# Kernel optimization log

Hardware: AMD Instinct MI355X
Metric: run time of the kernel (lower is better)

The kernel has to match this reference:

```python
import jax, jax.numpy as jnp
import numpy as np

B, DIM, RES, NS, ITERS = 64, 256, 32, 8, 5
NTOK = RES * RES
HID = max(DIM, 128)
EPS = 1e-08
SCALE = DIM ** -0.5


def build_grid(res):
    r = [np.linspace(0.0, 1.0, num=n) for n in (res, res)]
    g = np.stack(np.meshgrid(*r, sparse=False, indexing='ij'), axis=-1)
    g = g.reshape(1, res, res, 2).astype(np.float32)
    return jnp.asarray(np.concatenate([g, 1.0 - g], axis=-1))  # [1,res,res,4]


def ln(x, g, b, eps=1e-5):
    m = x.mean(-1, keepdims=True)
    v = ((x - m) ** 2).mean(-1, keepdims=True)
    return (x - m) / jnp.sqrt(v + eps) * g + b


def ln2(x, g, b, eps=1e-5):  # LayerNorm over last two dims ([ntokens, dim])
    m = x.mean((-2, -1), keepdims=True)
    v = ((x - m) ** 2).mean((-2, -1), keepdims=True)
    return (x - m) / jnp.sqrt(v + eps) * g + b


def lin(x, W, b):
    return x @ W.T + b


def gru_cell(x, h, W_ih, W_hh, b_ih, b_hh):
    gi = x @ W_ih.T + b_ih
    gh = h @ W_hh.T + b_hh
    ir, iz, i_n = jnp.split(gi, 3, axis=-1)
    hr, hz, h_n = jnp.split(gh, 3, axis=-1)
    r = jax.nn.sigmoid(ir + hr)
    z = jax.nn.sigmoid(iz + hz)
    n = jnp.tanh(i_n + r * h_n)
    return (1.0 - z) * n + z * h


def setup_inputs() -> dict:
    key = jax.random.key(0)
    ks = jax.random.split(key, 32)
    p = lambda i, shape, s=0.02: (jax.random.normal(ks[i], shape, dtype=jnp.float32) * s)
    d = {
        'inputs': jax.random.normal(ks[0], (B, DIM, RES, RES), dtype=jnp.float32),
        'init_noise': jax.random.normal(ks[1], (B, NS, DIM), dtype=jnp.float32),
        'W_pos': p(2, (DIM, 4)), 'b_pos': jnp.zeros((DIM,)),
        'g_enc': jnp.ones((NTOK, DIM)), 'b_enc': jnp.zeros((NTOK, DIM)),
        'W_m1': p(3, (DIM, DIM)), 'b_m1': jnp.zeros((DIM,)),
        'W_m2': p(4, (DIM, DIM)), 'b_m2': jnp.zeros((DIM,)),
        'g_in': jnp.ones((DIM,)), 'b_in': jnp.zeros((DIM,)),
        'Wq': p(5, (DIM, DIM)), 'bq': jnp.zeros((DIM,)),
        'Wk': p(6, (DIM, DIM)), 'bk': jnp.zeros((DIM,)),
        'Wv': p(7, (DIM, DIM)), 'bv': jnp.zeros((DIM,)),
        'W_ih': p(8, (3 * DIM, DIM)), 'W_hh': p(9, (3 * DIM, DIM)),
        'b_ih': jnp.zeros((3 * DIM,)), 'b_hh': jnp.zeros((3 * DIM,)),
        'g_s': jnp.ones((DIM,)), 'b_s': jnp.zeros((DIM,)),
        'g_ff': jnp.ones((DIM,)), 'b_ff': jnp.zeros((DIM,)),
        'W_f1': p(10, (HID, DIM)), 'b_f1': jnp.zeros((HID,)),
        'W_f2': p(11, (DIM, HID)), 'b_f2': jnp.zeros((DIM,)),
        'mu': p(12, (1, 1, DIM), 0.1), 'sigma': p(13, (1, 1, DIM), 0.1),
    }
    return d


def _forward(inputs, init_noise, W_pos, b_pos, g_enc, b_enc, W_m1, b_m1, W_m2, b_m2,
             g_in, b_in, Wq, bq, Wk, bk, Wv, bv, W_ih, W_hh, b_ih, b_hh,
             g_s, b_s, g_ff, b_ff, W_f1, b_f1, W_f2, b_f2, mu, sigma):
    grid = build_grid(RES)  # [1,RES,RES,4]
    # encoder transformation (position=True)
    f = jnp.transpose(inputs, (0, 2, 3, 1))               # [B,RES,RES,DIM]
    f = f + lin(grid, W_pos, b_pos)                       # soft position embed
    f = f.reshape(B, NTOK, DIM)
    f = ln2(f, g_enc, b_enc)                              # LayerNorm([ntokens, dim])
    f = jnp.maximum(lin(f, W_m1, b_m1), 0.0)
    f = jnp.maximum(lin(f, W_m2, b_m2), 0.0)
    f = ln(f, g_in, b_in)                                 # norm_input
    k = lin(f, Wk, bk)
    v = lin(f, Wv, bv)

    def step(slots):
        s = ln(slots, g_s, b_s)
        q = lin(s, Wq, bq)
        dots = jnp.einsum('bid,bjd->bij', q, k) * SCALE   # [B,NS,NTOK]
        attn = jax.nn.softmax(dots, axis=1) + EPS         # softmax over slots
        attn = attn / attn.sum(-1, keepdims=True)         # weighted mean
        upd = jnp.einsum('bij,bjd->bid', attn, v)
        ns = gru_cell(upd.reshape(-1, DIM), slots.reshape(-1, DIM),
                      W_ih, W_hh, b_ih, b_hh).reshape(B, NS, DIM)
        h = jnp.maximum(lin(ln(ns, g_ff, b_ff), W_f1, b_f1), 0.0)
        return ns + lin(h, W_f2, b_f2)

    slots = mu + sigma * init_noise
    for _ in range(ITERS):
        slots = step(slots)
    # implicit differentiation: one extra step through detached slots
    slots = step(jax.lax.stop_gradient(slots))
    return slots


def reference(inputs, init_noise, W_pos, b_pos, g_enc, b_enc, W_m1, b_m1, W_m2, b_m2,
              g_in, b_in, Wq, bq, Wk, bk, Wv, bv, W_ih, W_hh, b_ih, b_hh,
              g_s, b_s, g_ff, b_ff, W_f1, b_f1, W_f2, b_f2, mu, sigma):
    return _forward(inputs, init_noise, W_pos, b_pos, g_enc, b_enc, W_m1, b_m1, W_m2, b_m2,
                    g_in, b_in, Wq, bq, Wk, bk, Wv, bv, W_ih, W_hh, b_ih, b_hh,
                    g_s, b_s, g_ff, b_ff, W_f1, b_f1, W_f2, b_f2, mu, sigma)
```

## Files before the change

kernel.cpp:

```cpp
#include <hip/hip_runtime.h>
#include <hip/hip_bf16.h>

#define BB    64
#define DIMN  256
#define NSLOT 8
#define NTOKN 1024
#define NSTEP 6
#define SCALEF 0.0625f

typedef __attribute__((ext_vector_type(8))) short short8;
typedef __attribute__((ext_vector_type(8))) unsigned short ushort8;
typedef __attribute__((ext_vector_type(4))) unsigned short ushort4v;
typedef __attribute__((ext_vector_type(4))) float f32x4;

__device__ __forceinline__ float b2f(unsigned short u) {
  return __uint_as_float((unsigned)u << 16);
}
__device__ __forceinline__ unsigned short f2b(float f) {
  unsigned u = __float_as_uint(f);
  return (unsigned short)((u + 0x7FFFu + ((u >> 16) & 1u)) >> 16);
}

constexpr int kNConv = 31;
constexpr int kConvSizes[kNConv] = {
  131072, 1024, 256, 262144, 262144, 65536, 256, 65536, 256, 256, 256,
  65536, 256, 65536, 256, 65536, 256, 196608, 196608, 768, 768,
  256, 256, 256, 256, 65536, 256, 65536, 256, 256, 256
};
constexpr int kConvTotal = 1513984;

struct PtrPack { const void* p[kNConv]; };

__device__ __forceinline__ float ldin(const void* p, long i, int isbf) {
  if (isbf) return b2f(((const unsigned short*)p)[i]);
  return ((const float*)p)[i];
}

__global__ void detect_dtype(const void* gin, int* flag) {
  unsigned u = *(const unsigned*)gin;
  *flag = (u == 0x3F803F80u) ? 1 : 0;
}

__global__ __launch_bounds__(256) void convert_weights(PtrPack pk, const int* __restrict__ flag,
                                                       float* __restrict__ dst) {
  int idx = blockIdx.x * 256 + threadIdx.x;
  if (idx >= kConvTotal) return;
  int off = idx, a = 0;
  while (a < kNConv - 1 && off >= kConvSizes[a]) { off -= kConvSizes[a]; ++a; }
  dst[idx] = ldin(pk.p[a], off, *flag);
}

constexpr int kWN = 9;
constexpr int kWSize[kWN]  = {65536, 65536, 65536, 65536, 65536, 196608, 196608, 65536, 65536};
constexpr int kWSrc[kWN]   = {656640, 722432, 788736, 854528, 920320, 986112, 1182720, 1381888, 1447680};
constexpr int kWTotal = 851968;

__global__ __launch_bounds__(256) void convert_wbf16(const float* __restrict__ conv,
                                                     unsigned short* __restrict__ wbf) {
  int idx = blockIdx.x * 256 + threadIdx.x;
  if (idx >= kWTotal) return;
  int off = idx, m = 0;
  while (m < kWN - 1 && off >= kWSize[m]) { off -= kWSize[m]; ++m; }
  wbf[idx] = f2b(conv[kWSrc[m] + off]);
}

__global__ __launch_bounds__(256) void posembed_stats(
    const void* __restrict__ in0, const int* __restrict__ flag,
    const float* __restrict__ Wpos, const float* __restrict__ bpos,
    unsigned short* __restrict__ A, float* __restrict__ partials) {
  __shared__ float lds[64 * 65];
  __shared__ float red[8];
  const int tb = blockIdx.x, b = blockIdx.y, tid = threadIdx.x;
  const int t0 = tb * 64;
  const int isbf = *flag;
  float sum = 0.f, ss = 0.f;
  const int tg = tid & 7;
  const int dbase = tid >> 3;
  const int tloc = tg * 8;
  const int dq = tid & 15;
  const int trow = tid >> 4;
  for (int d0 = 0; d0 < DIMN; d0 += 64) {
    __syncthreads();
#pragma unroll
    for (int p = 0; p < 2; ++p) {
      int dd = dbase + p * 32;
      int d = d0 + dd;
      const float* wp = Wpos + d * 4;
      int tf = t0 + tloc;
      float gi = (float)(tf >> 5) * (1.f / 31.f);
      float gj0 = (float)(tf & 31) * (1.f / 31.f);
      float base = wp[0] * gi + wp[2] * (1.f - gi) + wp[1] * gj0 + wp[3] * (1.f - gj0) + bpos[d];
      float step = (wp[1] - wp[3]) * (1.f / 31.f);
      long gidx = ((long)b * DIMN + d) * NTOKN + tf;
      float v[8];
      if (isbf) {
        ushort8 raw = *(const ushort8*)((const unsigned short*)in0 + gidx);
#pragma unroll
        for (int j = 0; j < 8; ++j) v[j] = b2f(raw[j]);
      } else {
        const float* fp = (const float*)in0 + gidx;
        float4 a0 = *(const float4*)fp;
        float4 a1 = *(const float4*)(fp + 4);
        v[0] = a0.x; v[1] = a0.y; v[2] = a0.z; v[3] = a0.w;
        v[4] = a1.x; v[5] = a1.y; v[6] = a1.z; v[7] = a1.w;
      }
#pragma unroll
      for (int j = 0; j < 8; ++j) {
        float val = v[j] + base + step * (float)j;
        sum += val; ss += val * val;
        lds[dd * 65 + tloc + j] = val;
      }
    }
    __syncthreads();
#pragma unroll
    for (int p = 0; p < 4; ++p) {
      int tt = trow + p * 16;
      int dcol = dq * 4;
      ushort4v y;
      y[0] = f2b(lds[(dcol + 0) * 65 + tt]);
      y[1] = f2b(lds[(dcol + 1) * 65 + tt]);
      y[2] = f2b(lds[(dcol + 2) * 65 + tt]);
      y[3] = f2b(lds[(dcol + 3) * 65 + tt]);
      *(ushort4v*)(A + ((long)b * NTOKN + t0 + tt) * DIMN + d0 + dcol) = y;
    }
  }
  for (int off = 32; off; off >>= 1) { sum += __shfl_xor(sum, off); ss += __shfl_xor(ss, off); }
  int w = tid >> 6;
  if ((tid & 63) == 0) { red[w] = sum; red[4 + w] = ss; }
  __syncthreads();
  if (tid == 0) {
    partials[((long)b * 16 + tb) * 2]     = red[0] + red[1] + red[2] + red[3];
    partials[((long)b * 16 + tb) * 2 + 1] = red[4] + red[5] + red[6] + red[7];
  }
}

__global__ void stats_reduce(const float* __restrict__ partials, float* __restrict__ stats) {
  int b = threadIdx.x;
  if (b >= BB) return;
  float s = 0.f, q = 0.f;
  for (int i = 0; i < 16; ++i) {
    s += partials[((long)b * 16 + i) * 2];
    q += partials[((long)b * 16 + i) * 2 + 1];
  }
  const float invN = 1.f / (float)(NTOKN * DIMN);
  float m = s * invN;
  float var = q * invN - m * m;
  stats[b * 2] = m;
  stats[b * 2 + 1] = rsqrtf(var + 1e-5f);
}

__global__ __launch_bounds__(256) void ln2_apply(unsigned short* __restrict__ A, const float* __restrict__ stats,
                                                 const float* __restrict__ genc, const float* __restrict__ benc) {
  long i8 = (long)blockIdx.x * 256 + threadIdx.x;
  long i = i8 * 8;
  int b = (int)(i >> 18);
  int td = (int)(i & 262143);
  float m = stats[b * 2], inv = stats[b * 2 + 1];
  ushort8 x = *(const ushort8*)(A + i);
  ushort8 y;
#pragma unroll
  for (int e = 0; e < 8; ++e) {
    float v = (b2f(x[e]) - m) * inv * genc[td + e] + benc[td + e];
    y[e] = f2b(v);
  }
  *(ushort8*)(A + i) = y;
}

__global__ __launch_bounds__(256) void rowln_bf(const unsigned short* __restrict__ X,
                                                const float* __restrict__ g, const float* __restrict__ bb,
                                                unsigned short* __restrict__ Y) {
  const int tid = threadIdx.x, lane = tid & 63;
  const long row = (long)blockIdx.x * 4 + (tid >> 6);
  ushort4v xv = *(const ushort4v*)(X + row * 256 + lane * 4);
  float x0 = b2f(xv[0]), x1 = b2f(xv[1]), x2 = b2f(xv[2]), x3 = b2f(xv[3]);
  float s = x0 + x1 + x2 + x3;
  float q = x0 * x0 + x1 * x1 + x2 * x2 + x3 * x3;
  for (int off = 32; off; off >>= 1) { s += __shfl_xor(s, off); q += __shfl_xor(q, off); }
  float m = s * (1.f / 256.f);
  float inv = rsqrtf(q * (1.f / 256.f) - m * m + 1e-5f);
  float4 gv = *(const float4*)(g + lane * 4);
  float4 bv = *(const float4*)(bb + lane * 4);
  ushort4v y;
  y[0] = f2b((x0 - m) * inv * gv.x + bv.x);
  y[1] = f2b((x1 - m) * inv * gv.y + bv.y);
  y[2] = f2b((x2 - m) * inv * gv.z + bv.z);
  y[3] = f2b((x3 - m) * inv * gv.w + bv.w);
  *(ushort4v*)(Y + row * 256 + lane * 4) = y;
}

template <int ACT, int OUT>
__global__ __launch_bounds__(256) void gemm_tile(
    const unsigned short* __restrict__ X, const unsigned short* __restrict__ W,
    const float* __restrict__ bias, const float* __restrict__ res,
    void* __restrict__ Y, int Nfull) {
  __shared__ unsigned short As[128 * 264];
  __shared__ unsigned short Bs[128 * 264];
  const int tid = threadIdx.x;
  const long m0 = (long)blockIdx.x * 128;
  const int n0 = blockIdx.y * 128;
#pragma unroll
  for (int i = 0; i < 16; ++i) {
    int c = tid + i * 256;
    int row = c >> 5, seg = c & 31;
    *(ushort8*)&As[row * 264 + seg * 8] = *(const ushort8*)(X + (m0 + row) * 256 + seg * 8);
  }
#pragma unroll
  for (int i = 0; i < 16; ++i) {
    int c = tid + i * 256;
    int row = c >> 5, seg = c & 31;
    *(ushort8*)&Bs[row * 264 + seg * 8] = *(const ushort8*)(W + (long)(n0 + row) * 256 + seg * 8);
  }
  __syncthreads();
  const int wave = tid >> 6, lane = tid & 63;
  const int wr = wave >> 1, wc = wave & 1;
  const int lrow = lane & 15, kgrp = lane >> 4;
  f32x4 acc[4][4];
#pragma unroll
  for (int mt = 0; mt < 4; ++mt)
#pragma unroll
    for (int nt = 0; nt < 4; ++nt) acc[mt][nt] = f32x4{0.f, 0.f, 0.f, 0.f};
#pragma unroll
  for (int kc = 0; kc < 8; ++kc) {
    short8 af[4], bf[4];
#pragma unroll
    for (int mt = 0; mt < 4; ++mt)
      af[mt] = *(const short8*)&As[(wr * 64 + mt * 16 + lrow) * 264 + kc * 32 + kgrp * 8];
#pragma unroll
    for (int nt = 0; nt < 4; ++nt)
      bf[nt] = *(const short8*)&Bs[(wc * 64 + nt * 16 + lrow) * 264 + kc * 32 + kgrp * 8];
#pragma unroll
    for (int mt = 0; mt < 4; ++mt)
#pragma unroll
      for (int nt = 0; nt < 4; ++nt)
        acc[mt][nt] = __builtin_amdgcn_mfma_f32_16x16x32_bf16(af[mt], bf[nt], acc[mt][nt], 0, 0, 0);
  }
#pragma unroll
  for (int mt = 0; mt < 4; ++mt)
#pragma unroll
    for (int nt = 0; nt < 4; ++nt) {
      int n = n0 + wc * 64 + nt * 16 + lrow;
      float bn = bias[n];
#pragma unroll
      for (int r = 0; r < 4; ++r) {
        long m = m0 + wr * 64 + mt * 16 + kgrp * 4 + r;
        float v = acc[mt][nt][r] + bn;
        if (ACT) v = fmaxf(v, 0.f);
        if (OUT == 0)      ((unsigned short*)Y)[m * Nfull + n] = f2b(v);
        else if (OUT == 1) ((float*)Y)[m * Nfull + n] = v;
        else               ((float*)Y)[m * Nfull + n] = v + res[m * Nfull + n];
      }
    }
}

__global__ __launch_bounds__(256) void gemm_kv_tile(
    const unsigned short* __restrict__ X,
    const unsigned short* __restrict__ Wk, const unsigned short* __restrict__ Wv,
    const float* __restrict__ bk, const float* __restrict__ bv,
    unsigned short* __restrict__ Kb, unsigned short* __restrict__ Vb) {
  __shared__ unsigned short As[128 * 264];
  __shared__ unsigned short Bs[128 * 264];
  const int tid = threadIdx.x;
  const long m0 = (long)blockIdx.x * 128;
  const int n0 = blockIdx.y * 128;
#pragma unroll
  for (int i = 0; i < 16; ++i) {
    int c = tid + i * 256;
    int row = c >> 5, seg = c & 31;
    *(ushort8*)&As[row * 264 + seg * 8] = *(const ushort8*)(X + (m0 + row) * 256 + seg * 8);
  }
  const int wave = tid >> 6, lane = tid & 63;
  const int wr = wave >> 1, wc = wave & 1;
  const int lrow = lane & 15, kgrp = lane >> 4;
  for (int which = 0; which < 2; ++which) {
    const unsigned short* W = which ? Wv : Wk;
    const float* bias = which ? bv : bk;
    unsigned short* Y = which ? Vb : Kb;
    if (which) __syncthreads();
#pragma unroll
    for (int i = 0; i < 16; ++i) {
      int c = tid + i * 256;
      int row = c >> 5, seg = c & 31;
      *(ushort8*)&Bs[row * 264 + seg * 8] = *(const ushort8*)(W + (long)(n0 + row) * 256 + seg * 8);
    }
    __syncthreads();
    f32x4 acc[4][4];
#pragma unroll
    for (int mt = 0; mt < 4; ++mt)
#pragma unroll
      for (int nt = 0; nt < 4; ++nt) acc[mt][nt] = f32x4{0.f, 0.f, 0.f, 0.f};
#pragma unroll
    for (int kc = 0; kc < 8; ++kc) {
      short8 af[4], bf[4];
#pragma unroll
      for (int mt = 0; mt < 4; ++mt)
        af[mt] = *(const short8*)&As[(wr * 64 + mt * 16 + lrow) * 264 + kc * 32 + kgrp * 8];
#pragma unroll
      for (int nt = 0; nt < 4; ++nt)
        bf[nt] = *(const short8*)&Bs[(wc * 64 + nt * 16 + lrow) * 264 + kc * 32 + kgrp * 8];
#pragma unroll
      for (int mt = 0; mt < 4; ++mt)
#pragma unroll
        for (int nt = 0; nt < 4; ++nt)
          acc[mt][nt] = __builtin_amdgcn_mfma_f32_16x16x32_bf16(af[mt], bf[nt], acc[mt][nt], 0, 0, 0);
    }
#pragma unroll
    for (int mt = 0; mt < 4; ++mt)
#pragma unroll
      for (int nt = 0; nt < 4; ++nt) {
        int n = n0 + wc * 64 + nt * 16 + lrow;
        float bn = bias[n];
#pragma unroll
        for (int r = 0; r < 4; ++r) {
          long m = m0 + wr * 64 + mt * 16 + kgrp * 4 + r;
          Y[m * 256 + n] = f2b(acc[mt][nt][r] + bn);
        }
      }
  }
}

template <int ACT, int OUT>
__global__ __launch_bounds__(256) void gemm_tile64(
    const unsigned short* __restrict__ X, const unsigned short* __restrict__ W,
    const float* __restrict__ bias, const float* __restrict__ res,
    void* __restrict__ Y, int Nfull) {
  __shared__ unsigned short As[64 * 264];
  __shared__ unsigned short Bs[128 * 264];
  const int tid = threadIdx.x;
  const long m0 = (long)blockIdx.x * 64;
  const int n0 = blockIdx.y * 128;
#pragma unroll
  for (int i = 0; i < 8; ++i) {
    int c = tid + i * 256;
    int row = c >> 5, seg = c & 31;
    *(ushort8*)&As[row * 264 + seg * 8] = *(const ushort8*)(X + (m0 + row) * 256 + seg * 8);
  }
#pragma unroll
  for (int i = 0; i < 16; ++i) {
    int c = tid + i * 256;
    int row = c >> 5, seg = c & 31;
    *(ushort8*)&Bs[row * 264 + seg * 8] = *(const ushort8*)(W + (long)(n0 + row) * 256 + seg * 8);
  }
  __syncthreads();
  const int wave = tid >> 6, lane = tid & 63;
  const int lrow = lane & 15, kgrp = lane >> 4;
  f32x4 acc[8];
#pragma unroll
  for (int nt = 0; nt < 8; ++nt) acc[nt] = f32x4{0.f, 0.f, 0.f, 0.f};
#pragma unroll
  for (int kc = 0; kc < 8; ++kc) {
    short8 af = *(const short8*)&As[(wave * 16 + lrow) * 264 + kc * 32 + kgrp * 8];
#pragma unroll
    for (int nt = 0; nt < 8; ++nt) {
      short8 bf = *(const short8*)&Bs[(nt * 16 + lrow) * 264 + kc * 32 + kgrp * 8];
      acc[nt] = __builtin_amdgcn_mfma_f32_16x16x32_bf16(af, bf, acc[nt], 0, 0, 0);
    }
  }
#pragma unroll
  for (int nt = 0; nt < 8; ++nt) {
    int n = n0 + nt * 16 + lrow;
    float bn = bias[n];
#pragma unroll
    for (int r = 0; r < 4; ++r) {
      long m = m0 + wave * 16 + kgrp * 4 + r;
      float v = acc[nt][r] + bn;
      if (ACT) v = fmaxf(v, 0.f);
      if (OUT == 0)      ((unsigned short*)Y)[m * Nfull + n] = f2b(v);
      else if (OUT == 1) ((float*)Y)[m * Nfull + n] = v;
      else               ((float*)Y)[m * Nfull + n] = v + res[m * Nfull + n];
    }
  }
}

__global__ __launch_bounds__(256) void gigh_tile(
    const unsigned short* __restrict__ updb, const unsigned short* __restrict__ sbf,
    const unsigned short* __restrict__ Wih, const unsigned short* __restrict__ Whh,
    const float* __restrict__ bih, const float* __restrict__ bhh,
    float* __restrict__ gib, float* __restrict__ ghb) {
  const unsigned short* X = blockIdx.z ? sbf : updb;
  const unsigned short* W = blockIdx.z ? Whh : Wih;
  const float* bias = blockIdx.z ? bhh : bih;
  float* Y = blockIdx.z ? ghb : gib;
  __shared__ unsigned short As[128 * 264];
  __shared__ unsigned short Bs[128 * 264];
  const int tid = threadIdx.x;
  const long m0 = (long)blockIdx.x * 128;
  const int n0 = blockIdx.y * 128;
#pragma unroll
  for (int i = 0; i < 16; ++i) {
    int c = tid + i * 256;
    int row = c >> 5, seg = c & 31;
    *(ushort8*)&As[row * 264 + seg * 8] = *(const ushort8*)(X + (m0 + row) * 256 + seg * 8);
  }
#pragma unroll
  for (int i = 0; i < 16; ++i) {
    int c = tid + i * 256;
    int row = c >> 5, seg = c & 31;
    *(ushort8*)&Bs[row * 264 + seg * 8] = *(const ushort8*)(W + (long)(n0 + row) * 256 + seg * 8);
  }
  __syncthreads();
  const int wave = tid >> 6, lane = tid & 63;
  const int wr = wave >> 1, wc = wave & 1;
  const int lrow = lane & 15, kgrp = lane >> 4;
  f32x4 acc[4][4];
#pragma unroll
  for (int mt = 0; mt < 4; ++mt)
#pragma unroll
    for (int nt = 0; nt < 4; ++nt) acc[mt][nt] = f32x4{0.f, 0.f, 0.f, 0.f};
#pragma unroll
  for (int kc = 0; kc < 8; ++kc) {
    short8 af[4], bf[4];
#pragma unroll
    for (int mt = 0; mt < 4; ++mt)
      af[mt] = *(const short8*)&As[(wr * 64 + mt * 16 + lrow) * 264 + kc * 32 + kgrp * 8];
#pragma unroll
    for (int nt = 0; nt < 4; ++nt)
      bf[nt] = *(const short8*)&Bs[(wc * 64 + nt * 16 + lrow) * 264 + kc * 32 + kgrp * 8];
#pragma unroll
    for (int mt = 0; mt < 4; ++mt)
#pragma unroll
      for (int nt = 0; nt < 4; ++nt)
        acc[mt][nt] = __builtin_amdgcn_mfma_f32_16x16x32_bf16(af[mt], bf[nt], acc[mt][nt], 0, 0, 0);
  }
#pragma unroll
  for (int mt = 0; mt < 4; ++mt)
#pragma unroll
    for (int nt = 0; nt < 4; ++nt) {
      int n = n0 + wc * 64 + nt * 16 + lrow;
      float bn = bias[n];
#pragma unroll
      for (int r = 0; r < 4; ++r) {
        long m = m0 + wr * 64 + mt * 16 + kgrp * 4 + r;
        Y[m * 768 + n] = acc[mt][nt][r] + bn;
      }
    }
}

__global__ __launch_bounds__(256) void slots_init(const float* __restrict__ noise, const float* __restrict__ mu,
                                                  const float* __restrict__ sigma, float* __restrict__ slots) {
  long i = (long)blockIdx.x * 256 + threadIdx.x;
  int d = (int)(i & 255);
  slots[i] = mu[d] + sigma[d] * noise[i];
}

__global__ __launch_bounds__(256) void lnq_q(
    const float* __restrict__ slots, const float* __restrict__ gs, const float* __restrict__ bs,
    const unsigned short* __restrict__ Wq, const float* __restrict__ bq,
    unsigned short* __restrict__ qb, unsigned short* __restrict__ sbf) {
  __shared__ unsigned short S[16 * 264];
  const int b = blockIdx.x, tid = threadIdx.x;
  const int wave = tid >> 6, lane = tid & 63;
  for (int i = tid; i < 8 * 264; i += 256) S[8 * 264 + i] = 0;
#pragma unroll
  for (int rr = 0; rr < 2; ++rr) {
    int row = wave * 2 + rr;
    float4 xv = *(const float4*)(slots + ((long)b * 8 + row) * 256 + lane * 4);
    float s = xv.x + xv.y + xv.z + xv.w;
    float q = xv.x * xv.x + xv.y * xv.y + xv.z * xv.z + xv.w * xv.w;
    for (int off = 32; off; off >>= 1) { s += __shfl_xor(s, off); q += __shfl_xor(q, off); }
    float m = s * (1.f / 256.f);
    float inv = rsqrtf(q * (1.f / 256.f) - m * m + 1e-5f);
    float4 gv = *(const float4*)(gs + lane * 4);
    float4 bv = *(const float4*)(bs + lane * 4);
    ushort4v y, rb;
    y[0] = f2b((xv.x - m) * inv * gv.x + bv.x);
    y[1] = f2b((xv.y - m) * inv * gv.y + bv.y);
    y[2] = f2b((xv.z - m) * inv * gv.z + bv.z);
    y[3] = f2b((xv.w - m) * inv * gv.w + bv.w);
    rb[0] = f2b(xv.x); rb[1] = f2b(xv.y); rb[2] = f2b(xv.z); rb[3] = f2b(xv.w);
    *(ushort4v*)&S[row * 264 + lane * 4] = y;
    *(ushort4v*)(sbf + ((long)b * 8 + row) * 256 + lane * 4) = rb;
  }
  __syncthreads();
  const int lrow = lane & 15, kgrp = lane >> 4;
  short8 a[8];
#pragma unroll
  for (int kc = 0; kc < 8; ++kc)
    a[kc] = *(const short8*)&S[lrow * 264 + kc * 32 + kgrp * 8];
#pragma unroll
  for (int nt = 0; nt < 4; ++nt) {
    const int n = wave * 64 + nt * 16 + lrow;
    const unsigned short* wp = Wq + (long)n * 256 + kgrp * 8;
    f32x4 acc = {0.f, 0.f, 0.f, 0.f};
#pragma unroll
    for (int kc = 0; kc < 8; ++kc)
      acc = __builtin_amdgcn_mfma_f32_16x16x32_bf16(a[kc], *(const short8*)(wp + kc * 32), acc, 0, 0, 0);
    if (kgrp < 2) {
      float bn = bq[n];
#pragma unroll
      for (int r = 0; r < 4; ++r)
        qb[((long)b * 8 + kgrp * 4 + r) * 256 + n] = f2b(acc[r] + bn);
    }
  }
}

__global__ __launch_bounds__(256) void attn1b(
    const unsigned short* __restrict__ qb, const unsigned short* __restrict__ Kb,
    const unsigned short* __restrict__ Vb,
    float* __restrict__ upd_part, float* __restrict__ asum_part) {
  __shared__ unsigned short Ks[64 * 264];
  __shared__ unsigned short Qs[16 * 264];
  __shared__ float attnS[64 * 8];
  __shared__ float red[4 * 2048];
  const int jt = blockIdx.x, b = blockIdx.y, tid = threadIdx.x;
  const int wave = tid >> 6, lane = tid & 63;
#pragma unroll
  for (int i = 0; i < 8; ++i) {
    int c = tid + i * 256;
    int row = c >> 5, seg = c & 31;
    *(ushort8*)&Ks[row * 264 + seg * 8] =
        *(const ushort8*)(Kb + ((long)(b * NTOKN + jt * 64 + row)) * 256 + seg * 8);
  }
  {
    int row = tid >> 5, seg = tid & 31;
    *(ushort8*)&Qs[row * 264 + seg * 8] = *(const ushort8*)(qb + ((long)(b * 8 + row)) * 256 + seg * 8);
  }
  for (int i = tid; i < 8 * 264; i += 256) Qs[8 * 264 + i] = 0;
  __syncthreads();
  const int lrow = lane & 15, kgrp = lane >> 4;
  f32x4 acc = {0.f, 0.f, 0.f, 0.f};
#pragma unroll
  for (int kc = 0; kc < 8; ++kc) {
    short8 af = *(const short8*)&Ks[(wave * 16 + lrow) * 264 + kc * 32 + kgrp * 8];
    short8 qf = *(const short8*)&Qs[lrow * 264 + kc * 32 + kgrp * 8];
    acc = __builtin_amdgcn_mfma_f32_16x16x32_bf16(af, qf, acc, 0, 0, 0);
  }
  float t0[4], mx[4], e[4], sm[4];
#pragma unroll
  for (int r = 0; r < 4; ++r) { t0[r] = acc[r] * SCALEF; mx[r] = t0[r]; }
#pragma unroll
  for (int msk = 1; msk <= 4; msk <<= 1)
#pragma unroll
    for (int r = 0; r < 4; ++r) mx[r] = fmaxf(mx[r], __shfl_xor(mx[r], msk));
#pragma unroll
  for (int r = 0; r < 4; ++r) { e[r] = expf(t0[r] - mx[r]); sm[r] = e[r]; }
#pragma unroll
  for (int msk = 1; msk <= 4; msk <<= 1)
#pragma unroll
    for (int r = 0; r < 4; ++r) sm[r] += __shfl_xor(sm[r], msk);
  if (lrow < 8) {
#pragma unroll
    for (int r = 0; r < 4; ++r) {
      int jl = wave * 16 + kgrp * 4 + r;
      attnS[jl * 8 + lrow] = e[r] / sm[r] + 1e-8f;
    }
  }
  __syncthreads();
  {
    int s0 = wave * 2;
    float v0 = attnS[lane * 8 + s0], v1 = attnS[lane * 8 + s0 + 1];
    for (int off = 32; off; off >>= 1) { v0 += __shfl_xor(v0, off); v1 += __shfl_xor(v1, off); }
    if (lane == 0) {
      asum_part[((long)(b * 16 + jt)) * 8 + s0] = v0;
      asum_part[((long)(b * 16 + jt)) * 8 + s0 + 1] = v1;
    }
  }
  float au[8][4] = {};
  for (int jl = 0; jl < 16; ++jl) {
    int j = wave * 16 + jl;
    ushort4v v4 = *(const ushort4v*)(Vb + ((long)(b * NTOKN + jt * 64 + j)) * 256 + lane * 4);
    float v0 = b2f(v4[0]), v1 = b2f(v4[1]), v2 = b2f(v4[2]), v3 = b2f(v4[3]);
    float4 a01 = *(const float4*)&attnS[j * 8];
    float4 a23 = *(const float4*)&attnS[j * 8 + 4];
    float aw[8] = {a01.x, a01.y, a01.z, a01.w, a23.x, a23.y, a23.z, a23.w};
#pragma unroll
    for (int s = 0; s < 8; ++s) {
      au[s][0] += aw[s] * v0; au[s][1] += aw[s] * v1;
      au[s][2] += aw[s] * v2; au[s][3] += aw[s] * v3;
    }
  }
#pragma unroll
  for (int s = 0; s < 8; ++s)
    *(float4*)&red[wave * 2048 + s * 256 + lane * 4] = make_float4(au[s][0], au[s][1], au[s][2], au[s][3]);
  __syncthreads();
#pragma unroll
  for (int i = 0; i < 8; ++i) {
    int idx = tid + i * 256;
    float sum = red[idx] + red[2048 + idx] + red[4096 + idx] + red[6144 + idx];
    upd_part[((long)(b * 16 + jt)) * 2048 + idx] = sum;
  }
}

__global__ __launch_bounds__(256) void upd_reduce(
    const float* __restrict__ upd_part, const float* __restrict__ asum_part,
    unsigned short* __restrict__ updb) {
  const int bx = blockIdx.x;
  const int b = bx >> 3, s = bx & 7;
  const int tid = threadIdx.x;
  float as = 0.f;
#pragma unroll
  for (int jt = 0; jt < 16; ++jt) as += asum_part[((long)(b * 16 + jt)) * 8 + s];
  float sum = 0.f;
#pragma unroll
  for (int jt = 0; jt < 16; ++jt)
    sum += upd_part[((long)(b * 16 + jt)) * 2048 + s * 256 + tid];
  updb[((long)b * 8 + s) * 256 + tid] = f2b(sum / as);
}

__global__ __launch_bounds__(256) void gru_ln(const float* __restrict__ gi, const float* __restrict__ gh,
                                              const float* __restrict__ slots,
                                              const float* __restrict__ gff, const float* __restrict__ bff,
                                              float* __restrict__ ns, unsigned short* __restrict__ ffl) {
  const int tid = threadIdx.x, lane = tid & 63;
  const long row = (long)blockIdx.x * 4 + (tid >> 6);
  const int d = lane * 4;
  float4 i1 = *(const float4*)(gi + row * 768 + d);
  float4 i2 = *(const float4*)(gi + row * 768 + 256 + d);
  float4 i3 = *(const float4*)(gi + row * 768 + 512 + d);
  float4 h1 = *(const float4*)(gh + row * 768 + d);
  float4 h2 = *(const float4*)(gh + row * 768 + 256 + d);
  float4 h3 = *(const float4*)(gh + row * 768 + 512 + d);
  float4 sl = *(const float4*)(slots + row * 256 + d);
  float n4[4];
  float r, z, nn;
  r = 1.f / (1.f + expf(-(i1.x + h1.x))); z = 1.f / (1.f + expf(-(i2.x + h2.x)));
  nn = tanhf(i3.x + r * h3.x); n4[0] = (1.f - z) * nn + z * sl.x;
  r = 1.f / (1.f + expf(-(i1.y + h1.y))); z = 1.f / (1.f + expf(-(i2.y + h2.y)));
  nn = tanhf(i3.y + r * h3.y); n4[1] = (1.f - z) * nn + z * sl.y;
  r = 1.f / (1.f + expf(-(i1.z + h1.z))); z = 1.f / (1.f + expf(-(i2.z + h2.z)));
  nn = tanhf(i3.z + r * h3.z); n4[2] = (1.f - z) * nn + z * sl.z;
  r = 1.f / (1.f + expf(-(i1.w + h1.w))); z = 1.f / (1.f + expf(-(i2.w + h2.w)));
  nn = tanhf(i3.w + r * h3.w); n4[3] = (1.f - z) * nn + z * sl.w;
  *(float4*)(ns + row * 256 + d) = make_float4(n4[0], n4[1], n4[2], n4[3]);
  float s = n4[0] + n4[1] + n4[2] + n4[3];
  float q = n4[0] * n4[0] + n4[1] * n4[1] + n4[2] * n4[2] + n4[3] * n4[3];
  for (int off = 32; off; off >>= 1) { s += __shfl_xor(s, off); q += __shfl_xor(q, off); }
  float m = s * (1.f / 256.f);
  float inv = rsqrtf(q * (1.f / 256.f) - m * m + 1e-5f);
  float4 gv = *(const float4*)(gff + d);
  float4 bv = *(const float4*)(bff + d);
  ushort4v y;
  y[0] = f2b((n4[0] - m) * inv * gv.x + bv.x);
  y[1] = f2b((n4[1] - m) * inv * gv.y + bv.y);
  y[2] = f2b((n4[2] - m) * inv * gv.z + bv.z);
  y[3] = f2b((n4[3] - m) * inv * gv.w + bv.w);
  *(ushort4v*)(ffl + row * 256 + d) = y;
}

__global__ __launch_bounds__(256) void write_out(const float* __restrict__ slots, const int* __restrict__ flag,
                                                 void* __restrict__ out) {
  long i = (long)blockIdx.x * 256 + threadIdx.x;
  float v = slots[i];
  if (*flag) ((__hip_bfloat16*)out)[i] = __float2bfloat16(v);
  else ((float*)out)[i] = v;
}

extern "C" void kernel_launch(void* const* d_in, const int* in_sizes, int n_in,
                              void* d_out, int out_size, void* d_ws, size_t ws_size,
                              hipStream_t stream) {
  (void)in_sizes; (void)n_in; (void)out_size; (void)ws_size;
  float* wsf = (float*)d_ws;
  long o = 0;
  float* conv = wsf; o += kConvTotal;
  unsigned short* wbf = (unsigned short*)(wsf + o); o += kWTotal / 2;
  unsigned short* A   = (unsigned short*)(wsf + o); o += (long)BB * NTOKN * DIMN / 2;
  unsigned short* X1  = (unsigned short*)(wsf + o); o += (long)BB * NTOKN * DIMN / 2;
  unsigned short* X2  = (unsigned short*)(wsf + o); o += (long)BB * NTOKN * DIMN / 2;
  unsigned short* Kb  = (unsigned short*)(wsf + o); o += (long)BB * NTOKN * DIMN / 2;
  unsigned short* Vb  = (unsigned short*)(wsf + o); o += (long)BB * NTOKN * DIMN / 2;
  float* slots = wsf + o; o += 131072;
  unsigned short* sbf = (unsigned short*)(wsf + o); o += 65536;
  unsigned short* qb  = (unsigned short*)(wsf + o); o += 65536;
  float* upd_part = wsf + o; o += 2097152;
  float* asum_part = wsf + o; o += 8192;
  unsigned short* updb = (unsigned short*)(wsf + o); o += 65536;
  float* gib   = wsf + o; o += 393216;
  float* ghb   = wsf + o; o += 393216;
  float* nsb   = wsf + o; o += 131072;
  unsigned short* ffl  = (unsigned short*)(wsf + o); o += 65536;
  unsigned short* hbuf = (unsigned short*)(wsf + o); o += 65536;
  float* partials = wsf + o; o += 2048;
  float* stats = wsf + o; o += 128;
  int* flag = (int*)(wsf + o); o += 16;

  long coff[kNConv];
  { long acc = 0; for (int i = 0; i < kNConv; ++i) { coff[i] = acc; acc += kConvSizes[i]; } }
  const float* noise_f = conv + coff[0];
  const float* Wpos = conv + coff[1];
  const float* bpos = conv + coff[2];
  const float* genc = conv + coff[3];
  const float* benc = conv + coff[4];
  const float* bm1  = conv + coff[6];
  const float* bm2  = conv + coff[8];
  const float* gin  = conv + coff[9];
  const float* bin  = conv + coff[10];
  const float* bq   = conv + coff[12];
  const float* bk   = conv + coff[14];
  const float* bv   = conv + coff[16];
  const float* bih  = conv + coff[19];
  const float* bhh  = conv + coff[20];
  const float* gs   = conv + coff[21];
  const float* bs   = conv + coff[22];
  const float* gff  = conv + coff[23];
  const float* bff  = conv + coff[24];
  const float* bf1  = conv + coff[26];
  const float* bf2  = conv + coff[28];
  const float* mu   = conv + coff[29];
  const float* sigma = conv + coff[30];

  const unsigned short* Wm1b = wbf;
  const unsigned short* Wm2b = wbf + 65536;
  const unsigned short* Wqb  = wbf + 131072;
  const unsigned short* Wkb  = wbf + 196608;
  const unsigned short* Wvb  = wbf + 262144;
  const unsigned short* Wihb = wbf + 327680;
  const unsigned short* Whhb = wbf + 524288;
  const unsigned short* Wf1b = wbf + 720896;
  const unsigned short* Wf2b = wbf + 786432;

  detect_dtype<<<1, 1, 0, stream>>>(d_in[10], flag);

  PtrPack pk;
  for (int i = 0; i < kNConv; ++i) pk.p[i] = d_in[i + 1];
  convert_weights<<<(kConvTotal + 255) / 256, 256, 0, stream>>>(pk, flag, conv);
  convert_wbf16<<<(kWTotal + 255) / 256, 256, 0, stream>>>(conv, wbf);

  posembed_stats<<<dim3(16, 64), 256, 0, stream>>>(d_in[0], flag, Wpos, bpos, A, partials);
  stats_reduce<<<1, 64, 0, stream>>>(partials, stats);
  ln2_apply<<<8192, 256, 0, stream>>>(A, stats, genc, benc);
  const int MT = BB * NTOKN / 128;
  gemm_tile<1, 0><<<dim3(MT, 2), 256, 0, stream>>>(A,  Wm1b, bm1, nullptr, X1, 256);
  gemm_tile<1, 0><<<dim3(MT, 2), 256, 0, stream>>>(X1, Wm2b, bm2, nullptr, A,  256);
  rowln_bf<<<BB * NTOKN / 4, 256, 0, stream>>>(A, gin, bin, X2);
  gemm_kv_tile<<<dim3(MT, 2), 256, 0, stream>>>(X2, Wkb, Wvb, bk, bv, Kb, Vb);

  slots_init<<<512, 256, 0, stream>>>(noise_f, mu, sigma, slots);

  for (int it = 0; it < NSTEP; ++it) {
    lnq_q<<<64, 256, 0, stream>>>(slots, gs, bs, Wqb, bq, qb, sbf);
    attn1b<<<dim3(16, 64), 256, 0, stream>>>(qb, Kb, Vb, upd_part, asum_part);
    upd_reduce<<<512, 256, 0, stream>>>(upd_part, asum_part, updb);
    gigh_tile<<<dim3(4, 6, 2), 256, 0, stream>>>(updb, sbf, Wihb, Whhb, bih, bhh, gib, ghb);
    gru_ln<<<128, 256, 0, stream>>>(gib, ghb, slots, gff, bff, nsb, ffl);
    gemm_tile64<1, 0><<<dim3(8, 2), 256, 0, stream>>>(ffl, Wf1b, bf1, nullptr, hbuf, 256);
    gemm_tile64<0, 2><<<dim3(8, 2), 256, 0, stream>>>(hbuf, Wf2b, bf2, nsb, slots, 256);
  }

  write_out<<<512, 256, 0, stream>>>(slots, flag, d_out);
}
```

Baseline: 443.8 us.

## Fuse LN2 into MLP1 load, row LN into MLP2 epilogue, and FF1/FF2 into one kernel

Folds the encoder LayerNorm into the A-tile load of the first MLP GEMM and computes the per-row input LayerNorm inside a full-width (N=256) second MLP GEMM epilogue. This removes two elementwise passes over the large token tensor and their extra round trips through global memory. It also fuses the two slot feed-forward GEMMs into a single kernel that keeps the hidden activation in LDS, dropping one launch per iteration. In exchange, the MLP1 load now reads fp32 gamma/beta per element, and the fused kernels launch fewer blocks (8 blocks for the FF kernel), which lowers parallelism.

```diff
diff --git a/kernel.cpp b/kernel.cpp
--- a/kernel.cpp
+++ b/kernel.cpp
@@ -149,60 +149,32 @@
   stats[b * 2 + 1] = rsqrtf(var + 1e-5f);
 }
 
-__global__ __launch_bounds__(256) void ln2_apply(unsigned short* __restrict__ A, const float* __restrict__ stats,
-                                                 const float* __restrict__ genc, const float* __restrict__ benc) {
-  long i8 = (long)blockIdx.x * 256 + threadIdx.x;
-  long i = i8 * 8;
-  int b = (int)(i >> 18);
-  int td = (int)(i & 262143);
-  float m = stats[b * 2], inv = stats[b * 2 + 1];
-  ushort8 x = *(const ushort8*)(A + i);
-  ushort8 y;
-#pragma unroll
-  for (int e = 0; e < 8; ++e) {
-    float v = (b2f(x[e]) - m) * inv * genc[td + e] + benc[td + e];
-    y[e] = f2b(v);
-  }
-  *(ushort8*)(A + i) = y;
-}
-
-__global__ __launch_bounds__(256) void rowln_bf(const unsigned short* __restrict__ X,
-                                                const float* __restrict__ g, const float* __restrict__ bb,
-                                                unsigned short* __restrict__ Y) {
-  const int tid = threadIdx.x, lane = tid & 63;
-  const long row = (long)blockIdx.x * 4 + (tid >> 6);
-  ushort4v xv = *(const ushort4v*)(X + row * 256 + lane * 4);
-  float x0 = b2f(xv[0]), x1 = b2f(xv[1]), x2 = b2f(xv[2]), x3 = b2f(xv[3]);
-  float s = x0 + x1 + x2 + x3;
-  float q = x0 * x0 + x1 * x1 + x2 * x2 + x3 * x3;
-  for (int off = 32; off; off >>= 1) { s += __shfl_xor(s, off); q += __shfl_xor(q, off); }
-  float m = s * (1.f / 256.f);
-  float inv = rsqrtf(q * (1.f / 256.f) - m * m + 1e-5f);
-  float4 gv = *(const float4*)(g + lane * 4);
-  float4 bv = *(const float4*)(bb + lane * 4);
-  ushort4v y;
-  y[0] = f2b((x0 - m) * inv * gv.x + bv.x);
-  y[1] = f2b((x1 - m) * inv * gv.y + bv.y);
-  y[2] = f2b((x2 - m) * inv * gv.z + bv.z);
-  y[3] = f2b((x3 - m) * inv * gv.w + bv.w);
-  *(ushort4v*)(Y + row * 256 + lane * 4) = y;
-}
-
-template <int ACT, int OUT>
-__global__ __launch_bounds__(256) void gemm_tile(
-    const unsigned short* __restrict__ X, const unsigned short* __restrict__ W,
-    const float* __restrict__ bias, const float* __restrict__ res,
-    void* __restrict__ Y, int Nfull) {
+__global__ __launch_bounds__(256) void gemm_m1ln(
+    const unsigned short* __restrict__ X, const float* __restrict__ stats,
+    const float* __restrict__ genc, const float* __restrict__ benc,
+    const unsigned short* __restrict__ W, const float* __restrict__ bias,
+    unsigned short* __restrict__ Y) {
   __shared__ unsigned short As[128 * 264];
   __shared__ unsigned short Bs[128 * 264];
   const int tid = threadIdx.x;
   const long m0 = (long)blockIdx.x * 128;
   const int n0 = blockIdx.y * 128;
+  const int bb_ = (int)(m0 >> 10);
+  const float mm = stats[bb_ * 2], inv = stats[bb_ * 2 + 1];
 #pragma unroll
   for (int i = 0; i < 16; ++i) {
     int c = tid + i * 256;
     int row = c >> 5, seg = c & 31;
-    *(ushort8*)&As[row * 264 + seg * 8] = *(const ushort8*)(X + (m0 + row) * 256 + seg * 8);
+    long grow = m0 + row;
+    int t = (int)(grow & 1023);
+    ushort8 raw = *(const ushort8*)(X + grow * 256 + seg * 8);
+    const float* gp = genc + (long)t * 256 + seg * 8;
+    const float* bp = benc + (long)t * 256 + seg * 8;
+    ushort8 y;
+#pragma unroll
+    for (int e = 0; e < 8; ++e)
+      y[e] = f2b((b2f(raw[e]) - mm) * inv * gp[e] + bp[e]);
+    *(ushort8*)&As[row * 264 + seg * 8] = y;
   }
 #pragma unroll
   for (int i = 0; i < 16; ++i) {
@@ -243,13 +215,82 @@
 #pragma unroll
       for (int r = 0; r < 4; ++r) {
         long m = m0 + wr * 64 + mt * 16 + kgrp * 4 + r;
-        float v = acc[mt][nt][r] + bn;
-        if (ACT) v = fmaxf(v, 0.f);
-        if (OUT == 0)      ((unsigned short*)Y)[m * Nfull + n] = f2b(v);
-        else if (OUT == 1) ((float*)Y)[m * Nfull + n] = v;
-        else               ((float*)Y)[m * Nfull + n] = v + res[m * Nfull + n];
-      }
-    }
+        Y[m * 256 + n] = f2b(fmaxf(acc[mt][nt][r] + bn, 0.f));
+      }
+    }
+}
+
+__global__ __launch_bounds__(256) void gemm_m2ln_tile(
+    const unsigned short* __restrict__ X, const unsigned short* __restrict__ W,
+    const float* __restrict__ bias, const float* __restrict__ gin, const float* __restrict__ bin,
+    unsigned short* __restrict__ Y) {
+  __shared__ unsigned short As[64 * 264];
+  __shared__ unsigned short Bs[128 * 264];
+  const int tid = threadIdx.x;
+  const long m0 = (long)blockIdx.x * 64;
+#pragma unroll
+  for (int i = 0; i < 8; ++i) {
+    int c = tid + i * 256;
+    int row = c >> 5, seg = c & 31;
+    *(ushort8*)&As[row * 264 + seg * 8] = *(const ushort8*)(X + (m0 + row) * 256 + seg * 8);
+  }
+  const int wave = tid >> 6, lane = tid & 63;
+  const int lrow = lane & 15, kgrp = lane >> 4;
+  f32x4 vals[16];
+  short8 a[8];
+  for (int half = 0; half < 2; ++half) {
+    if (half) __syncthreads();
+#pragma unroll
+    for (int i = 0; i < 16; ++i) {
+      int c = tid + i * 256;
+      int row = c >> 5, seg = c & 31;
+      *(ushort8*)&Bs[row * 264 + seg * 8] = *(const ushort8*)(W + (long)(half * 128 + row) * 256 + seg * 8);
+    }
+    __syncthreads();
+    if (!half)
+#pragma unroll
+      for (int kc = 0; kc < 8; ++kc)
+        a[kc] = *(const short8*)&As[(wave * 16 + lrow) * 264 + kc * 32 + kgrp * 8];
+#pragma unroll
+    for (int nt = 0; nt < 8; ++nt) {
+      f32x4 acc = {0.f, 0.f, 0.f, 0.f};
+#pragma unroll
+      for (int kc = 0; kc < 8; ++kc) {
+        short8 bf = *(const short8*)&Bs[(nt * 16 + lrow) * 264 + kc * 32 + kgrp * 8];
+        acc = __builtin_amdgcn_mfma_f32_16x16x32_bf16(a[kc], bf, acc, 0, 0, 0);
+      }
+      int n = half * 128 + nt * 16 + lrow;
+      float bn = bias[n];
+#pragma unroll
+      for (int r = 0; r < 4; ++r) acc[r] = fmaxf(acc[r] + bn, 0.f);
+      vals[half * 8 + nt] = acc;
+    }
+  }
+  float sr[4] = {0.f, 0.f, 0.f, 0.f}, qr[4] = {0.f, 0.f, 0.f, 0.f};
+#pragma unroll
+  for (int j = 0; j < 16; ++j)
+#pragma unroll
+    for (int r = 0; r < 4; ++r) { float v = vals[j][r]; sr[r] += v; qr[r] += v * v; }
+#pragma unroll
+  for (int msk = 1; msk <= 8; msk <<= 1)
+#pragma unroll
+    for (int r = 0; r < 4; ++r) { sr[r] += __shfl_xor(sr[r], msk); qr[r] += __shfl_xor(qr[r], msk); }
+  float mean[4], invr[4];
+#pragma unroll
+  for (int r = 0; r < 4; ++r) {
+    mean[r] = sr[r] * (1.f / 256.f);
+    invr[r] = rsqrtf(qr[r] * (1.f / 256.f) - mean[r] * mean[r] + 1e-5f);
+  }
+#pragma unroll
+  for (int j = 0; j < 16; ++j) {
+    int n = (j >> 3) * 128 + (j & 7) * 16 + lrow;
+    float gn = gin[n], bn2 = bin[n];
+#pragma unroll
+    for (int r = 0; r < 4; ++r) {
+      long m = m0 + wave * 16 + kgrp * 4 + r;
+      Y[m * 256 + n] = f2b((vals[j][r] - mean[r]) * invr[r] * gn + bn2);
+    }
+  }
 }
 
 __global__ __launch_bounds__(256) void gemm_kv_tile(
@@ -315,59 +356,6 @@
           Y[m * 256 + n] = f2b(acc[mt][nt][r] + bn);
         }
       }
-  }
-}
-
-template <int ACT, int OUT>
-__global__ __launch_bounds__(256) void gemm_tile64(
-    const unsigned short* __restrict__ X, const unsigned short* __restrict__ W,
-    const float* __restrict__ bias, const float* __restrict__ res,
-    void* __restrict__ Y, int Nfull) {
-  __shared__ unsigned short As[64 * 264];
-  __shared__ unsigned short Bs[128 * 264];
-  const int tid = threadIdx.x;
-  const long m0 = (long)blockIdx.x * 64;
-  const int n0 = blockIdx.y * 128;
-#pragma unroll
-  for (int i = 0; i < 8; ++i) {
-    int c = tid + i * 256;
-    int row = c >> 5, seg = c & 31;
-    *(ushort8*)&As[row * 264 + seg * 8] = *(const ushort8*)(X + (m0 + row) * 256 + seg * 8);
-  }
-#pragma unroll
-  for (int i = 0; i < 16; ++i) {
-    int c = tid + i * 256;
-    int row = c >> 5, seg = c & 31;
-    *(ushort8*)&Bs[row * 264 + seg * 8] = *(const ushort8*)(W + (long)(n0 + row) * 256 + seg * 8);
-  }
-  __syncthreads();
-  const int wave = tid >> 6, lane = tid & 63;
-  const int lrow = lane & 15, kgrp = lane >> 4;
-  f32x4 acc[8];
-#pragma unroll
-  for (int nt = 0; nt < 8; ++nt) acc[nt] = f32x4{0.f, 0.f, 0.f, 0.f};
-#pragma unroll
-  for (int kc = 0; kc < 8; ++kc) {
-    short8 af = *(const short8*)&As[(wave * 16 + lrow) * 264 + kc * 32 + kgrp * 8];
-#pragma unroll
-    for (int nt = 0; nt < 8; ++nt) {
-      short8 bf = *(const short8*)&Bs[(nt * 16 + lrow) * 264 + kc * 32 + kgrp * 8];
-      acc[nt] = __builtin_amdgcn_mfma_f32_16x16x32_bf16(af, bf, acc[nt], 0, 0, 0);
-    }
-  }
-#pragma unroll
-  for (int nt = 0; nt < 8; ++nt) {
-    int n = n0 + nt * 16 + lrow;
-    float bn = bias[n];
-#pragma unroll
-    for (int r = 0; r < 4; ++r) {
-      long m = m0 + wave * 16 + kgrp * 4 + r;
-      float v = acc[nt][r] + bn;
-      if (ACT) v = fmaxf(v, 0.f);
-      if (OUT == 0)      ((unsigned short*)Y)[m * Nfull + n] = f2b(v);
-      else if (OUT == 1) ((float*)Y)[m * Nfull + n] = v;
-      else               ((float*)Y)[m * Nfull + n] = v + res[m * Nfull + n];
-    }
   }
 }
 
@@ -433,6 +421,101 @@
         Y[m * 768 + n] = acc[mt][nt][r] + bn;
       }
     }
+}
+
+__global__ __launch_bounds__(256) void ff12_tile(
+    const unsigned short* __restrict__ X,
+    const unsigned short* __restrict__ W1, const float* __restrict__ b1,
+    const unsigned short* __restrict__ W2, const float* __restrict__ b2,
+    const float* __restrict__ res, float* __restrict__ out) {
+  __shared__ unsigned short As[64 * 264];
+  __shared__ unsigned short Bs[128 * 264];
+  const int tid = threadIdx.x;
+  const long m0 = (long)blockIdx.x * 64;
+#pragma unroll
+  for (int i = 0; i < 8; ++i) {
+    int c = tid + i * 256;
+    int row = c >> 5, seg = c & 31;
+    *(ushort8*)&As[row * 264 + seg * 8] = *(const ushort8*)(X + (m0 + row) * 256 + seg * 8);
+  }
+  const int wave = tid >> 6, lane = tid & 63;
+  const int lrow = lane & 15, kgrp = lane >> 4;
+  f32x4 vals[16];
+  {
+    short8 a[8];
+    for (int half = 0; half < 2; ++half) {
+      if (half) __syncthreads();
+#pragma unroll
+      for (int i = 0; i < 16; ++i) {
+        int c = tid + i * 256;
+        int row = c >> 5, seg = c & 31;
+        *(ushort8*)&Bs[row * 264 + seg * 8] = *(const ushort8*)(W1 + (long)(half * 128 + row) * 256 + seg * 8);
+      }
+      __syncthreads();
+      if (!half)
+#pragma unroll
+        for (int kc = 0; kc < 8; ++kc)
+          a[kc] = *(const short8*)&As[(wave * 16 + lrow) * 264 + kc * 32 + kgrp * 8];
+#pragma unroll
+      for (int nt = 0; nt < 8; ++nt) {
+        f32x4 acc = {0.f, 0.f, 0.f, 0.f};
+#pragma unroll
+        for (int kc = 0; kc < 8; ++kc) {
+          short8 bf = *(const short8*)&Bs[(nt * 16 + lrow) * 264 + kc * 32 + kgrp * 8];
+          acc = __builtin_amdgcn_mfma_f32_16x16x32_bf16(a[kc], bf, acc, 0, 0, 0);
+        }
+        int n = half * 128 + nt * 16 + lrow;
+        float bn = b1[n];
+#pragma unroll
+        for (int r = 0; r < 4; ++r) acc[r] = fmaxf(acc[r] + bn, 0.f);
+        vals[half * 8 + nt] = acc;
+      }
+    }
+  }
+  __syncthreads();
+#pragma unroll
+  for (int j = 0; j < 16; ++j) {
+    int n = (j >> 3) * 128 + (j & 7) * 16 + lrow;
+#pragma unroll
+    for (int r = 0; r < 4; ++r) {
+      int row = wave * 16 + kgrp * 4 + r;
+      As[row * 264 + n] = f2b(vals[j][r]);
+    }
+  }
+  __syncthreads();
+  {
+    short8 a[8];
+    for (int half = 0; half < 2; ++half) {
+      if (half) __syncthreads();
+#pragma unroll
+      for (int i = 0; i < 16; ++i) {
+        int c = tid + i * 256;
+        int row = c >> 5, seg = c & 31;
+        *(ushort8*)&Bs[row * 264 + seg * 8] = *(const ushort8*)(W2 + (long)(half * 128 + row) * 256 + seg * 8);
+      }
+      __syncthreads();
+      if (!half)
+#pragma unroll
+        for (int kc = 0; kc < 8; ++kc)
+          a[kc] = *(const short8*)&As[(wave * 16 + lrow) * 264 + kc * 32 + kgrp * 8];
+#pragma unroll
+      for (int nt = 0; nt < 8; ++nt) {
+        f32x4 acc = {0.f, 0.f, 0.f, 0.f};
+#pragma unroll
+        for (int kc = 0; kc < 8; ++kc) {
+          short8 bf = *(const short8*)&Bs[(nt * 16 + lrow) * 264 + kc * 32 + kgrp * 8];
+          acc = __builtin_amdgcn_mfma_f32_16x16x32_bf16(a[kc], bf, acc, 0, 0, 0);
+        }
+        int n = half * 128 + nt * 16 + lrow;
+        float bn = b2[n];
+#pragma unroll
+        for (int r = 0; r < 4; ++r) {
+          long m = m0 + wave * 16 + kgrp * 4 + r;
+          out[m * 256 + n] = acc[r] + bn + res[m * 256 + n];
+        }
+      }
+    }
+  }
 }
 
 __global__ __launch_bounds__(256) void slots_init(const float* __restrict__ noise, const float* __restrict__ mu,
@@ -667,7 +750,6 @@
   float* ghb   = wsf + o; o += 393216;
   float* nsb   = wsf + o; o += 131072;
   unsigned short* ffl  = (unsigned short*)(wsf + o); o += 65536;
-  unsigned short* hbuf = (unsigned short*)(wsf + o); o += 65536;
   float* partials = wsf + o; o += 2048;
   float* stats = wsf + o; o += 128;
   int* flag = (int*)(wsf + o); o += 16;
@@ -716,11 +798,9 @@
 
   posembed_stats<<<dim3(16, 64), 256, 0, stream>>>(d_in[0], flag, Wpos, bpos, A, partials);
   stats_reduce<<<1, 64, 0, stream>>>(partials, stats);
-  ln2_apply<<<8192, 256, 0, stream>>>(A, stats, genc, benc);
   const int MT = BB * NTOKN / 128;
-  gemm_tile<1, 0><<<dim3(MT, 2), 256, 0, stream>>>(A,  Wm1b, bm1, nullptr, X1, 256);
-  gemm_tile<1, 0><<<dim3(MT, 2), 256, 0, stream>>>(X1, Wm2b, bm2, nullptr, A,  256);
-  rowln_bf<<<BB * NTOKN / 4, 256, 0, stream>>>(A, gin, bin, X2);
+  gemm_m1ln<<<dim3(MT, 2), 256, 0, stream>>>(A, stats, genc, benc, Wm1b, bm1, X1);
+  gemm_m2ln_tile<<<BB * NTOKN / 64, 256, 0, stream>>>(X1, Wm2b, bm2, gin, bin, X2);
   gemm_kv_tile<<<dim3(MT, 2), 256, 0, stream>>>(X2, Wkb, Wvb, bk, bv, Kb, Vb);
 
   slots_init<<<512, 256, 0, stream>>>(noise_f, mu, sigma, slots);
@@ -731,8 +811,7 @@
     upd_reduce<<<512, 256, 0, stream>>>(upd_part, asum_part, updb);
     gigh_tile<<<dim3(4, 6, 2), 256, 0, stream>>>(updb, sbf, Wihb, Whhb, bih, bhh, gib, ghb);
     gru_ln<<<128, 256, 0, stream>>>(gib, ghb, slots, gff, bff, nsb, ffl);
-    gemm_tile64<1, 0><<<dim3(8, 2), 256, 0, stream>>>(ffl, Wf1b, bf1, nullptr, hbuf, 256);
-    gemm_tile64<0, 2><<<dim3(8, 2), 256, 0, stream>>>(hbuf, Wf2b, bf2, nsb, slots, 256);
+    ff12_tile<<<8, 256, 0, stream>>>(ffl, Wf1b, bf1, Wf2b, bf2, nsb, slots);
   }
 
   write_out<<<512, 256, 0, stream>>>(slots, flag, d_out);
```

New measurement: 497.4 us. +12.1%, slower.
